# Optimization experiments

Hardware: AMD Instinct MI355X
Metric: run time of the kernel (lower is better)

Reference implementation:

```python
import jax, jax.numpy as jnp
import numpy as np

N, T = 32, 1024
CIN, H, O, F2 = 64, 128, 16, 16  # F2 = 2 * FiLMed_layers
EPS = 1e-5
SLOPE = 0.01  # nn.LeakyReLU default


def _leaky(x):
    return jnp.where(x >= 0, x, SLOPE * x)


def _ln(x, gamma, beta):
    # x: (N,T,O,H); gamma,beta: (O,H) -> broadcast per channel
    mu = jnp.mean(x, axis=-1, keepdims=True)
    var = jnp.mean(jnp.square(x - mu), axis=-1, keepdims=True)
    return (x - mu) * jax.lax.rsqrt(var + EPS) * gamma + beta


def setup_inputs() -> dict:
    key = jax.random.key(0)
    ks = jax.random.split(key, 7)
    s0 = 1.0 / np.sqrt(CIN)
    s1 = 1.0 / np.sqrt(H)
    return {
        "x": jax.random.normal(ks[0], (N, T, CIN), jnp.float32),
        "W0": jax.random.uniform(ks[1], (O, H, CIN), jnp.float32, -s0, s0),
        "b0": jax.random.uniform(ks[2], (O, H), jnp.float32, -s0, s0),
        "g0": jnp.ones((O, H), jnp.float32),
        "be0": jnp.zeros((O, H), jnp.float32),
        "W1": jax.random.uniform(ks[3], (O, H, H), jnp.float32, -s1, s1),
        "b1": jax.random.uniform(ks[4], (O, H), jnp.float32, -s1, s1),
        "g1": jnp.ones((O, H), jnp.float32),
        "be1": jnp.zeros((O, H), jnp.float32),
        "W2": jax.random.uniform(ks[5], (O, F2, H), jnp.float32, -s1, s1),
        "b2": jax.random.uniform(ks[6], (O, F2), jnp.float32, -s1, s1),
    }


def reference(x, W0, b0, g0, be0, W1, b1, g1, be1, W2, b2):
    # Per-channel MLP, vectorized over the O channel axis.
    h = jnp.einsum("ntc,ohc->ntoh", x, W0) + b0          # (N,T,O,H)
    h = _ln(_leaky(h), g0, be0)
    h = jnp.einsum("ntoh,ogh->ntog", h, W1) + b1         # (N,T,O,H)
    h = _ln(_leaky(h), g1, be1)
    out = jnp.einsum("ntoh,ofh->ntof", h, W2) + b2       # (N,T,O,F2)
    out = _leaky(out)
    # torch: stack(dim=1) -> (N,O,T,F2); moveaxis(1,-1) -> (N,T,F2,O)
    return jnp.moveaxis(out, 2, 3)
```

## Files before the change

kernel.cpp:

```cpp
#include <hip/hip_runtime.h>

#define NTOK  32768
#define CIN   64
#define HDIM  128
#define O_CH  16
#define F2    16
#define SLOPE 0.01f
#define EPS   1e-5f

#define SW0_STRIDE 72
#define SW1_STRIDE 136
#define SW2_STRIDE 136
#define SH_STRIDE  136
#define SW0_OFF 0
#define SW1_OFF 9216
#define SW2_OFF (9216 + 17408)
#define WIMG_SHORTS 28800
#define SH_OFF  28800
#define SMEM_TOT (28800 + 64 * SH_STRIDE)

#define WIMG_OFF   0
#define WIMG_BYTES ((size_t)O_CH * WIMG_SHORTS * 2)
#define XBF_OFF    WIMG_BYTES
#define XBF_BYTES  ((size_t)NTOK * CIN * 2)
#define B0F_OFF    (XBF_OFF + XBF_BYTES)
#define B0F_BYTES  ((size_t)O_CH * HDIM * 4)
#define B1F_OFF    (B0F_OFF + B0F_BYTES)
#define B1F_BYTES  ((size_t)O_CH * HDIM * 4)
#define B2F_OFF    (B1F_OFF + B1F_BYTES)
#define B2F_BYTES  ((size_t)O_CH * F2 * 4)

typedef __attribute__((ext_vector_type(8))) short bf16x8;
typedef __attribute__((ext_vector_type(4))) short bf16x4;
typedef __attribute__((ext_vector_type(4))) float f32x4;

__device__ __forceinline__ float b2f(unsigned short u) {
  union { unsigned int i; float f; } v;
  v.i = ((unsigned int)u) << 16;
  return v.f;
}
__device__ __forceinline__ unsigned short f2b(float f) {
  union { float f; unsigned int i; } v;
  v.f = f;
  unsigned int i = v.i;
  unsigned int r = (i + 0x7fffu + ((i >> 16) & 1u)) >> 16;
  return (unsigned short)r;
}
__device__ __forceinline__ float leaky(float t) {
  return (t >= 0.f) ? t : SLOPE * t;
}
__device__ __forceinline__ bf16x8 cvt8(const float* __restrict__ p) {
  float4 a = *(const float4*)p;
  float4 b = *(const float4*)(p + 4);
  bf16x8 r;
  r[0] = (short)f2b(a.x); r[1] = (short)f2b(a.y);
  r[2] = (short)f2b(a.z); r[3] = (short)f2b(a.w);
  r[4] = (short)f2b(b.x); r[5] = (short)f2b(b.y);
  r[6] = (short)f2b(b.z); r[7] = (short)f2b(b.w);
  return r;
}
__device__ __forceinline__ bf16x8 cvt8s(const float* __restrict__ p,
                                        const float* __restrict__ s) {
  bf16x8 r;
#pragma unroll
  for (int i = 0; i < 8; ++i) r[i] = (short)f2b(p[i] * s[i]);
  return r;
}

__device__ __forceinline__ void leaky_ln_store(
    const f32x4* acc, unsigned short* __restrict__ sh,
    int row0, int lo16, int quad) {
  float v[8][4];
  float s1 = 0.f, s2 = 0.f;
#pragma unroll
  for (int nt = 0; nt < 8; ++nt) {
#pragma unroll
    for (int r = 0; r < 4; ++r) {
      float t = leaky(acc[nt][r]);
      v[nt][r] = t;
      s1 += t;
      s2 += t * t;
    }
  }
  s1 += __shfl_xor(s1, 16); s2 += __shfl_xor(s2, 16);
  s1 += __shfl_xor(s1, 32); s2 += __shfl_xor(s2, 32);
  float mu = s1 * (1.0f / 128.0f);
  float var = s2 * (1.0f / 128.0f) - mu * mu;
  float rs = rsqrtf(var + EPS);
#pragma unroll
  for (int nt = 0; nt < 8; ++nt) {
    bf16x4 p;
#pragma unroll
    for (int r = 0; r < 4; ++r)
      p[r] = (short)f2b((v[nt][r] - mu) * rs);
    *(bf16x4*)&sh[(row0 + lo16) * SH_STRIDE + nt * 16 + quad * 4] = p;
  }
}

__global__ __launch_bounds__(256) void prep(
    const float* __restrict__ x,
    const float* __restrict__ W0, const float* __restrict__ b0,
    const float* __restrict__ g0, const float* __restrict__ be0,
    const float* __restrict__ W1, const float* __restrict__ b1,
    const float* __restrict__ g1, const float* __restrict__ be1,
    const float* __restrict__ W2, const float* __restrict__ b2,
    unsigned short* __restrict__ wimg, unsigned short* __restrict__ xbf,
    float* __restrict__ b0f, float* __restrict__ b1f,
    float* __restrict__ b2f) {
  const int bid = blockIdx.x, tid = threadIdx.x;
  if (bid < 16) {
    const int o = bid;
    __shared__ float sg0[HDIM], sbe0[HDIM], sg1[HDIM], sbe1[HDIM];
    if (tid < 128) {
      sg0[tid]  = g0 [o * HDIM + tid];
      sbe0[tid] = be0[o * HDIM + tid];
      sg1[tid]  = g1 [o * HDIM + tid];
      sbe1[tid] = be1[o * HDIM + tid];
    }
    __syncthreads();
    unsigned short* img = wimg + (size_t)o * WIMG_SHORTS;
    const float* w0 = W0 + (size_t)o * HDIM * CIN;
    for (int c = tid; c < (HDIM * CIN) / 8; c += 256) {
      int n = c >> 3, k8 = c & 7;
      *(bf16x8*)&img[SW0_OFF + n * SW0_STRIDE + k8 * 8] = cvt8(w0 + c * 8);
    }
    const float* w1 = W1 + (size_t)o * HDIM * HDIM;
    for (int c = tid; c < (HDIM * HDIM) / 8; c += 256) {
      int n = c >> 4, k8 = c & 15;
      *(bf16x8*)&img[SW1_OFF + n * SW1_STRIDE + k8 * 8] =
          cvt8s(w1 + c * 8, sg0 + k8 * 8);
    }
    const float* w2 = W2 + (size_t)o * F2 * HDIM;
    for (int c = tid; c < (F2 * HDIM) / 8; c += 256) {
      int n = c >> 4, k8 = c & 15;
      *(bf16x8*)&img[SW2_OFF + n * SW2_STRIDE + k8 * 8] =
          cvt8s(w2 + c * 8, sg1 + k8 * 8);
    }
    if (tid < 128) {
      b0f[o * HDIM + tid] = b0[o * HDIM + tid];
      float d = 0.f;
      const float* w1r = w1 + (size_t)tid * HDIM;
      for (int k = 0; k < HDIM; ++k) d += w1r[k] * sbe0[k];
      b1f[o * HDIM + tid] = b1[o * HDIM + tid] + d;
    } else if (tid < 144) {
      int f = tid - 128;
      float d = 0.f;
      const float* w2r = w2 + (size_t)f * HDIM;
      for (int k = 0; k < HDIM; ++k) d += w2r[k] * sbe1[k];
      b2f[o * F2 + f] = b2[o * F2 + f] + d;
    }
  } else {
    int idx = (bid - 16) * 256 + tid;
    *(bf16x8*)&xbf[(size_t)idx * 8] = cvt8(x + (size_t)idx * 8);
  }
}

__global__ __launch_bounds__(256, 2) void film_main(
    const unsigned short* __restrict__ xbf,
    const unsigned short* __restrict__ wimg,
    const float* __restrict__ b0f, const float* __restrict__ b1f,
    const float* __restrict__ b2f,
    float* __restrict__ out) {
  __shared__ unsigned short smem[SMEM_TOT];
  const int tid = threadIdx.x;
  const int c   = blockIdx.x & 7;
  const int o   = (blockIdx.x >> 3) & 15;
  const int q   = blockIdx.x >> 7;
  const int tok0 = (q * 8 + c) * 256;

  {
    const bf16x8* src = (const bf16x8*)(wimg + (size_t)o * WIMG_SHORTS);
    for (int i = tid; i < WIMG_SHORTS / 8; i += 256)
      *(bf16x8*)&smem[i * 8] = src[i];
  }

  const int lane = tid & 63;
  const int wave = tid >> 6;
  const int lo16 = lane & 15;
  const int quad = lane >> 4;
  const int row0 = wave * 16;

  f32x4 bias0[8], bias1[8];
#pragma unroll
  for (int nt = 0; nt < 8; ++nt) {
    bias0[nt] = *(const f32x4*)&b0f[o * HDIM + nt * 16 + quad * 4];
    bias1[nt] = *(const f32x4*)&b1f[o * HDIM + nt * 16 + quad * 4];
  }
  const f32x4 bias2 = *(const f32x4*)&b2f[o * F2 + quad * 4];
  __syncthreads();

  for (int mt = 0; mt < 4; ++mt) {
    const int trow = tok0 + wave * 64 + mt * 16;

    f32x4 acc[8];
#pragma unroll
    for (int nt = 0; nt < 8; ++nt) acc[nt] = bias0[nt];
    {
      const unsigned short* xr = xbf + (size_t)(trow + lo16) * CIN + quad * 8;
#pragma unroll
      for (int ks = 0; ks < 2; ++ks) {
        bf16x8 bx = *(const bf16x8*)(xr + ks * 32);
#pragma unroll
        for (int nt = 0; nt < 8; ++nt) {
          bf16x8 a = *(const bf16x8*)
              &smem[SW0_OFF + (nt * 16 + lo16) * SW0_STRIDE + ks * 32 + quad * 8];
          acc[nt] = __builtin_amdgcn_mfma_f32_16x16x32_bf16(a, bx, acc[nt], 0, 0, 0);
        }
      }
    }
    leaky_ln_store(acc, smem + SH_OFF, row0, lo16, quad);

#pragma unroll
    for (int nt = 0; nt < 8; ++nt) acc[nt] = bias1[nt];
#pragma unroll
    for (int ks = 0; ks < 4; ++ks) {
      bf16x8 bh = *(const bf16x8*)
          &smem[SH_OFF + (row0 + lo16) * SH_STRIDE + ks * 32 + quad * 8];
#pragma unroll
      for (int nt = 0; nt < 8; ++nt) {
        bf16x8 a = *(const bf16x8*)
            &smem[SW1_OFF + (nt * 16 + lo16) * SW1_STRIDE + ks * 32 + quad * 8];
        acc[nt] = __builtin_amdgcn_mfma_f32_16x16x32_bf16(a, bh, acc[nt], 0, 0, 0);
      }
    }
    leaky_ln_store(acc, smem + SH_OFF, row0, lo16, quad);

    f32x4 acc2 = bias2;
#pragma unroll
    for (int ks = 0; ks < 4; ++ks) {
      bf16x8 bh = *(const bf16x8*)
          &smem[SH_OFF + (row0 + lo16) * SH_STRIDE + ks * 32 + quad * 8];
      bf16x8 a = *(const bf16x8*)
          &smem[SW2_OFF + lo16 * SW2_STRIDE + ks * 32 + quad * 8];
      acc2 = __builtin_amdgcn_mfma_f32_16x16x32_bf16(a, bh, acc2, 0, 0, 0);
    }
    {
      const size_t tb = (size_t)(trow + lo16) * (F2 * O_CH);
#pragma unroll
      for (int r = 0; r < 4; ++r)
        out[tb + (quad * 4 + r) * O_CH + o] = leaky(acc2[r]);
    }
  }
}

extern "C" void kernel_launch(void* const* d_in, const int* in_sizes, int n_in,
                              void* d_out, int out_size, void* d_ws, size_t ws_size,
                              hipStream_t stream) {
  (void)in_sizes; (void)n_in; (void)out_size; (void)ws_size;
  const float* x   = (const float*)d_in[0];
  const float* W0  = (const float*)d_in[1];
  const float* b0  = (const float*)d_in[2];
  const float* g0  = (const float*)d_in[3];
  const float* be0 = (const float*)d_in[4];
  const float* W1  = (const float*)d_in[5];
  const float* b1  = (const float*)d_in[6];
  const float* g1  = (const float*)d_in[7];
  const float* be1 = (const float*)d_in[8];
  const float* W2  = (const float*)d_in[9];
  const float* b2  = (const float*)d_in[10];

  unsigned short* wimg = (unsigned short*)((char*)d_ws + WIMG_OFF);
  unsigned short* xbf  = (unsigned short*)((char*)d_ws + XBF_OFF);
  float* b0f = (float*)((char*)d_ws + B0F_OFF);
  float* b1f = (float*)((char*)d_ws + B1F_OFF);
  float* b2f = (float*)((char*)d_ws + B2F_OFF);

  prep<<<dim3(16 + (NTOK * CIN / 8) / 256), dim3(256), 0, stream>>>(
      x, W0, b0, g0, be0, W1, b1, g1, be1, W2, b2, wimg, xbf, b0f, b1f, b2f);
  film_main<<<dim3(O_CH * (NTOK / 256)), dim3(256), 0, stream>>>(
      xbf, wimg, b0f, b1f, b2f, (float*)d_out);
}
```

Before: 171.3 us.

## Fuse x bf16 conversion into main kernel and use 1024-thread blocks

Drops the separate x-to-bf16 pass and its workspace buffer, so the main kernel reads fp32 x directly and converts it in registers before the first MFMA. Main-kernel blocks grow from 256 to 1024 threads, each covering 1024 tokens, so the per-channel weight image is loaded into LDS once per 1024 tokens rather than once per 256. The LDS hidden buffer grows to 256 rows to match. In exchange, occupancy drops to one large block per CU, launch bounds no longer request two blocks per SM, and x is read as fp32, doubling its bytes.

```diff
diff --git a/kernel.cpp b/kernel.cpp
--- a/kernel.cpp
+++ b/kernel.cpp
@@ -17,18 +17,16 @@
 #define SW2_OFF (9216 + 17408)
 #define WIMG_SHORTS 28800
 #define SH_OFF  28800
-#define SMEM_TOT (28800 + 64 * SH_STRIDE)
+#define SH_ROWS 256
+#define SMEM_SHORTS (28800 + SH_ROWS * SH_STRIDE)
 
 #define WIMG_OFF   0
 #define WIMG_BYTES ((size_t)O_CH * WIMG_SHORTS * 2)
-#define XBF_OFF    WIMG_BYTES
-#define XBF_BYTES  ((size_t)NTOK * CIN * 2)
-#define B0F_OFF    (XBF_OFF + XBF_BYTES)
+#define B0F_OFF    WIMG_BYTES
 #define B0F_BYTES  ((size_t)O_CH * HDIM * 4)
 #define B1F_OFF    (B0F_OFF + B0F_BYTES)
 #define B1F_BYTES  ((size_t)O_CH * HDIM * 4)
 #define B2F_OFF    (B1F_OFF + B1F_BYTES)
-#define B2F_BYTES  ((size_t)O_CH * F2 * 4)
 
 typedef __attribute__((ext_vector_type(8))) short bf16x8;
 typedef __attribute__((ext_vector_type(4))) short bf16x4;
@@ -98,79 +96,72 @@
 }
 
 __global__ __launch_bounds__(256) void prep(
-    const float* __restrict__ x,
     const float* __restrict__ W0, const float* __restrict__ b0,
     const float* __restrict__ g0, const float* __restrict__ be0,
     const float* __restrict__ W1, const float* __restrict__ b1,
     const float* __restrict__ g1, const float* __restrict__ be1,
     const float* __restrict__ W2, const float* __restrict__ b2,
-    unsigned short* __restrict__ wimg, unsigned short* __restrict__ xbf,
+    unsigned short* __restrict__ wimg,
     float* __restrict__ b0f, float* __restrict__ b1f,
     float* __restrict__ b2f) {
-  const int bid = blockIdx.x, tid = threadIdx.x;
-  if (bid < 16) {
-    const int o = bid;
-    __shared__ float sg0[HDIM], sbe0[HDIM], sg1[HDIM], sbe1[HDIM];
-    if (tid < 128) {
-      sg0[tid]  = g0 [o * HDIM + tid];
-      sbe0[tid] = be0[o * HDIM + tid];
-      sg1[tid]  = g1 [o * HDIM + tid];
-      sbe1[tid] = be1[o * HDIM + tid];
-    }
-    __syncthreads();
-    unsigned short* img = wimg + (size_t)o * WIMG_SHORTS;
-    const float* w0 = W0 + (size_t)o * HDIM * CIN;
-    for (int c = tid; c < (HDIM * CIN) / 8; c += 256) {
-      int n = c >> 3, k8 = c & 7;
-      *(bf16x8*)&img[SW0_OFF + n * SW0_STRIDE + k8 * 8] = cvt8(w0 + c * 8);
-    }
-    const float* w1 = W1 + (size_t)o * HDIM * HDIM;
-    for (int c = tid; c < (HDIM * HDIM) / 8; c += 256) {
-      int n = c >> 4, k8 = c & 15;
-      *(bf16x8*)&img[SW1_OFF + n * SW1_STRIDE + k8 * 8] =
-          cvt8s(w1 + c * 8, sg0 + k8 * 8);
-    }
-    const float* w2 = W2 + (size_t)o * F2 * HDIM;
-    for (int c = tid; c < (F2 * HDIM) / 8; c += 256) {
-      int n = c >> 4, k8 = c & 15;
-      *(bf16x8*)&img[SW2_OFF + n * SW2_STRIDE + k8 * 8] =
-          cvt8s(w2 + c * 8, sg1 + k8 * 8);
-    }
-    if (tid < 128) {
-      b0f[o * HDIM + tid] = b0[o * HDIM + tid];
-      float d = 0.f;
-      const float* w1r = w1 + (size_t)tid * HDIM;
-      for (int k = 0; k < HDIM; ++k) d += w1r[k] * sbe0[k];
-      b1f[o * HDIM + tid] = b1[o * HDIM + tid] + d;
-    } else if (tid < 144) {
-      int f = tid - 128;
-      float d = 0.f;
-      const float* w2r = w2 + (size_t)f * HDIM;
-      for (int k = 0; k < HDIM; ++k) d += w2r[k] * sbe1[k];
-      b2f[o * F2 + f] = b2[o * F2 + f] + d;
-    }
-  } else {
-    int idx = (bid - 16) * 256 + tid;
-    *(bf16x8*)&xbf[(size_t)idx * 8] = cvt8(x + (size_t)idx * 8);
-  }
-}
-
-__global__ __launch_bounds__(256, 2) void film_main(
-    const unsigned short* __restrict__ xbf,
+  const int o = blockIdx.x, tid = threadIdx.x;
+  __shared__ float sg0[HDIM], sbe0[HDIM], sg1[HDIM], sbe1[HDIM];
+  if (tid < 128) {
+    sg0[tid]  = g0 [o * HDIM + tid];
+    sbe0[tid] = be0[o * HDIM + tid];
+    sg1[tid]  = g1 [o * HDIM + tid];
+    sbe1[tid] = be1[o * HDIM + tid];
+  }
+  __syncthreads();
+  unsigned short* img = wimg + (size_t)o * WIMG_SHORTS;
+  const float* w0 = W0 + (size_t)o * HDIM * CIN;
+  for (int c = tid; c < (HDIM * CIN) / 8; c += 256) {
+    int n = c >> 3, k8 = c & 7;
+    *(bf16x8*)&img[SW0_OFF + n * SW0_STRIDE + k8 * 8] = cvt8(w0 + c * 8);
+  }
+  const float* w1 = W1 + (size_t)o * HDIM * HDIM;
+  for (int c = tid; c < (HDIM * HDIM) / 8; c += 256) {
+    int n = c >> 4, k8 = c & 15;
+    *(bf16x8*)&img[SW1_OFF + n * SW1_STRIDE + k8 * 8] =
+        cvt8s(w1 + c * 8, sg0 + k8 * 8);
+  }
+  const float* w2 = W2 + (size_t)o * F2 * HDIM;
+  for (int c = tid; c < (F2 * HDIM) / 8; c += 256) {
+    int n = c >> 4, k8 = c & 15;
+    *(bf16x8*)&img[SW2_OFF + n * SW2_STRIDE + k8 * 8] =
+        cvt8s(w2 + c * 8, sg1 + k8 * 8);
+  }
+  if (tid < 128) {
+    b0f[o * HDIM + tid] = b0[o * HDIM + tid];
+    float d = 0.f;
+    const float* w1r = w1 + (size_t)tid * HDIM;
+    for (int k = 0; k < HDIM; ++k) d += w1r[k] * sbe0[k];
+    b1f[o * HDIM + tid] = b1[o * HDIM + tid] + d;
+  } else if (tid < 144) {
+    int f = tid - 128;
+    float d = 0.f;
+    const float* w2r = w2 + (size_t)f * HDIM;
+    for (int k = 0; k < HDIM; ++k) d += w2r[k] * sbe1[k];
+    b2f[o * F2 + f] = b2[o * F2 + f] + d;
+  }
+}
+
+__global__ __launch_bounds__(1024) void film_main(
+    const float* __restrict__ x,
     const unsigned short* __restrict__ wimg,
     const float* __restrict__ b0f, const float* __restrict__ b1f,
     const float* __restrict__ b2f,
     float* __restrict__ out) {
-  __shared__ unsigned short smem[SMEM_TOT];
+  __shared__ unsigned short smem[SMEM_SHORTS];
   const int tid = threadIdx.x;
   const int c   = blockIdx.x & 7;
   const int o   = (blockIdx.x >> 3) & 15;
   const int q   = blockIdx.x >> 7;
-  const int tok0 = (q * 8 + c) * 256;
+  const int tok0 = (q * 8 + c) * 1024;
 
   {
     const bf16x8* src = (const bf16x8*)(wimg + (size_t)o * WIMG_SHORTS);
-    for (int i = tid; i < WIMG_SHORTS / 8; i += 256)
+    for (int i = tid; i < WIMG_SHORTS / 8; i += 1024)
       *(bf16x8*)&smem[i * 8] = src[i];
   }
 
@@ -196,10 +187,10 @@
 #pragma unroll
     for (int nt = 0; nt < 8; ++nt) acc[nt] = bias0[nt];
     {
-      const unsigned short* xr = xbf + (size_t)(trow + lo16) * CIN + quad * 8;
+      const float* xr = x + (size_t)(trow + lo16) * CIN + quad * 8;
 #pragma unroll
       for (int ks = 0; ks < 2; ++ks) {
-        bf16x8 bx = *(const bf16x8*)(xr + ks * 32);
+        bf16x8 bx = cvt8(xr + ks * 32);
 #pragma unroll
         for (int nt = 0; nt < 8; ++nt) {
           bf16x8 a = *(const bf16x8*)
@@ -260,13 +251,12 @@
   const float* b2  = (const float*)d_in[10];
 
   unsigned short* wimg = (unsigned short*)((char*)d_ws + WIMG_OFF);
-  unsigned short* xbf  = (unsigned short*)((char*)d_ws + XBF_OFF);
   float* b0f = (float*)((char*)d_ws + B0F_OFF);
   float* b1f = (float*)((char*)d_ws + B1F_OFF);
   float* b2f = (float*)((char*)d_ws + B2F_OFF);
 
-  prep<<<dim3(16 + (NTOK * CIN / 8) / 256), dim3(256), 0, stream>>>(
-      x, W0, b0, g0, be0, W1, b1, g1, be1, W2, b2, wimg, xbf, b0f, b1f, b2f);
-  film_main<<<dim3(O_CH * (NTOK / 256)), dim3(256), 0, stream>>>(
-      xbf, wimg, b0f, b1f, b2f, (float*)d_out);
-}
+  prep<<<dim3(O_CH), dim3(256), 0, stream>>>(
+      W0, b0, g0, be0, W1, b1, g1, be1, W2, b2, wimg, b0f, b1f, b2f);
+  film_main<<<dim3(O_CH * (NTOK / 1024)), dim3(1024), 0, stream>>>(
+      x, wimg, b0f, b1f, b2f, (float*)d_out);
+}
```

New measurement: 174.7 us. About the same (+2.0%).
